# Performance work log

Measured on AMD Instinct MI355X. Metric: run time of the kernel, lower is better.

## Reference

```python
import jax, jax.numpy as jnp
import numpy as np


def setup_inputs() -> dict:
    key = jax.random.key(0)
    k1, k2 = jax.random.split(key)
    b, n, d = 8, 4096, 512
    num_codebooks, codebook_size = 1, 8192
    x = jax.random.normal(k1, (b, n, d), dtype=jnp.float32)
    embed = jax.random.normal(k2, (num_codebooks, codebook_size, d), dtype=jnp.float32)
    return {"x": x, "embed": embed}


def reference(x, embed):
    # Eval-mode forward of EuclideanCodebook (temperature 0 -> argmax of -cdist).
    # x: [b, n, d]; embed: [h, C, d] with h = num_codebooks = 1.
    b, n, d = x.shape
    h, C, _ = embed.shape
    flatten = x.reshape(h, b * n, d)                       # h * d packing (h=1)

    # dist = -cdist(flatten, embed): negative euclidean distance [h, N, C]
    x2 = jnp.sum(flatten * flatten, axis=-1, keepdims=True)   # [h, N, 1]
    e2 = jnp.sum(embed * embed, axis=-1)[:, None, :]          # [h, 1, C]
    xe = jnp.einsum('hnd,hcd->hnc', flatten, embed)           # [h, N, C]
    d2 = jnp.clip(x2 + e2 - 2.0 * xe, 0.0)
    dist = -jnp.sqrt(d2)                                      # [h, N, C]

    # gumbel_sample at temp 0 / eval -> straight argmax
    embed_ind_flat = jnp.argmax(dist, axis=-1)                # [h, N]

    # quantize = batched_embedding(embed_ind, embed): gather codes
    quantize = jnp.take_along_axis(embed, embed_ind_flat[..., None], axis=1)  # [h, N, d]

    # unpack + drop the codebook dim (needs_codebook_dim path)
    quantize = quantize.reshape(b, n, d)
    embed_ind = embed_ind_flat.reshape(b, n)
    dist = dist.reshape(h, b, n, C)  # dist keeps the codebook dim, as in source
    return quantize, embed_ind, dist
```

## Files before the change

kernel.cpp:

```cpp
#include <hip/hip_runtime.h>
#include <hip/hip_fp16.h>
#include <stdint.h>

typedef _Float16 f16x8 __attribute__((ext_vector_type(8)));
typedef _Float16 f16x4 __attribute__((ext_vector_type(4)));
typedef float    f32x4 __attribute__((ext_vector_type(4)));

static constexpr int NROWS = 32768;
static constexpr int NCODE = 8192;
static constexpr int DDIM  = 512;
static constexpr int BM = 256, BN = 256, BK = 64;
static constexpr int NBM = NROWS / BM;
static constexpr int NBN = NCODE / BN;
static constexpr int NPART = NBN * 2;

static constexpr size_t OFF_IND  = (size_t)NROWS * DDIM;
static constexpr size_t OFF_DIST = OFF_IND + NROWS;

static constexpr size_t WS_XH   = 0;
static constexpr size_t WS_XL   = WS_XH + (size_t)NROWS * DDIM * 2;
static constexpr size_t WS_EH   = WS_XL + (size_t)NROWS * DDIM * 2;
static constexpr size_t WS_EL   = WS_EH + (size_t)NCODE * DDIM * 2;
static constexpr size_t WS_X2   = WS_EL + (size_t)NCODE * DDIM * 2;
static constexpr size_t WS_E2   = WS_X2 + (size_t)NROWS * 4;
static constexpr size_t WS_PART = WS_E2 + (size_t)NCODE * 4;

__device__ inline void gload_lds16(const void* g, void* l) {
  __builtin_amdgcn_global_load_lds((const __attribute__((address_space(1))) void*)g,
                                   (__attribute__((address_space(3))) void*)l,
                                   16, 0, 0);
}

__global__ __launch_bounds__(128)
void prep_kernel(const float* __restrict__ x, const float* __restrict__ e,
                 _Float16* __restrict__ xh, _Float16* __restrict__ xl,
                 _Float16* __restrict__ eh, _Float16* __restrict__ el,
                 float* __restrict__ x2, float* __restrict__ e2)
{
  int bid = blockIdx.x;
  const float* src; _Float16 *dh, *dl; float* nrm;
  if (bid < NROWS) {
    src = x + (size_t)bid * DDIM;
    dh = xh + (size_t)bid * DDIM;  dl = xl + (size_t)bid * DDIM;
    nrm = x2 + bid;
  } else {
    int r = bid - NROWS;
    src = e + (size_t)r * DDIM;
    dh = eh + (size_t)r * DDIM;    dl = el + (size_t)r * DDIM;
    nrm = e2 + r;
  }
  int t = threadIdx.x;
  float4 v = reinterpret_cast<const float4*>(src)[t];
  double s = (double)v.x*v.x + (double)v.y*v.y + (double)v.z*v.z + (double)v.w*v.w;
  f16x4 h, l;
  h.x = (_Float16)v.x; l.x = (_Float16)(v.x - (float)h.x);
  h.y = (_Float16)v.y; l.y = (_Float16)(v.y - (float)h.y);
  h.z = (_Float16)v.z; l.z = (_Float16)(v.z - (float)h.z);
  h.w = (_Float16)v.w; l.w = (_Float16)(v.w - (float)h.w);
  reinterpret_cast<f16x4*>(dh)[t] = h;
  reinterpret_cast<f16x4*>(dl)[t] = l;
  #pragma unroll
  for (int m = 1; m < 64; m <<= 1) s += __shfl_xor(s, m);
  __shared__ double sh[2];
  if ((t & 63) == 0) sh[t >> 6] = s;
  __syncthreads();
  if (t == 0) nrm[0] = (float)(sh[0] + sh[1]);
}

#define BARx __builtin_amdgcn_s_barrier()
#define VMC(n)  asm volatile("s_waitcnt vmcnt(" #n ")" ::: "memory")

__device__ __forceinline__ void MMX(f32x4 (&ac)[2][4], const f16x8 (&af)[2][2],
                                    const f16x8 (&bf)[4][2]) {
  __builtin_amdgcn_s_setprio(1);
  #pragma unroll
  for (int m = 0; m < 2; ++m)
    #pragma unroll
    for (int n = 0; n < 4; ++n)
      #pragma unroll
      for (int ks = 0; ks < 2; ++ks)
        ac[m][n] = __builtin_amdgcn_mfma_f32_16x16x32_f16(af[m][ks], bf[n][ks], ac[m][n], 0, 0, 0);
  __builtin_amdgcn_s_setprio(0);
}

__global__ __launch_bounds__(512, 1)
void dist_gemm_kernel(const _Float16* __restrict__ xh, const _Float16* __restrict__ xl,
                      const _Float16* __restrict__ eh, const _Float16* __restrict__ el,
                      const float* __restrict__ x2, const float* __restrict__ e2,
                      float* __restrict__ dist, float2* __restrict__ part)
{
  __shared__ _Float16 L[2][2][BM * BK];

  const int tid  = threadIdx.x;
  const int wid  = tid >> 6;
  const int lane = tid & 63;
  const int qwr  = wid >> 1;
  const int qwc  = wid & 1;

  const int flat = blockIdx.x;
  const int xcd  = flat & 7;
  const int idx  = flat >> 3;
  const int bn   = xcd * 4 + (idx & 3);
  const int bm   = idx >> 2;
  const int R  = bm * BM;
  const int Cc = bn * BN;

  const int l3 = lane >> 3;
  const int l7 = lane & 7;
  const int srcslot = ((l7 ^ l3) << 4);

  auto STAGE_HALF = [&](int t, int nb, int half) {
    const int ab = half & 1;
    const int hh = half >> 1;
    const _Float16* base;
    size_t rowbase;
    if (ab == 0) { base = (t < 16) ? xh : xl;              rowbase = (size_t)R;  }
    else         { base = (t < 8 || t >= 16) ? eh : el;    rowbase = (size_t)Cc; }
    const int k0b = (t & 7) * (BK * 2);
    #pragma unroll
    for (int i = 0; i < 2; ++i) {
      const int rr = hh * 128 + wid * 16 + i * 8;
      gload_lds16((const char*)base + (rowbase + rr + l3) * (DDIM * 2) + k0b + srcslot,
                  &L[nb][ab][rr * BK]);
    }
  };

  const int l15   = lane & 15;
  const int kslot = (lane >> 4) << 4;

  auto LDA = [&](f16x8 (&af)[2][2], int b, int mq) {
    #pragma unroll
    for (int m = 0; m < 2; ++m)
      #pragma unroll
      for (int ks = 0; ks < 2; ++ks) {
        const int row = mq * 128 + qwr * 32 + m * 16 + l15;
        const int kb  = (ks * 64 + kslot) ^ ((row & 7) << 4);
        af[m][ks] = *(const f16x8*)((const char*)&L[b][0][0] + row * 128 + kb);
      }
  };
  auto LDB = [&](f16x8 (&bf)[4][2], int b, int nq) {
    #pragma unroll
    for (int n = 0; n < 4; ++n)
      #pragma unroll
      for (int ks = 0; ks < 2; ++ks) {
        const int row = nq * 128 + qwc * 64 + n * 16 + l15;
        const int kb  = (ks * 64 + kslot) ^ ((row & 7) << 4);
        bf[n][ks] = *(const f16x8*)((const char*)&L[b][1][0] + row * 128 + kb);
      }
  };

  f32x4 acc[2][2][2][4] = {};

  STAGE_HALF(0, 0, 0);
  STAGE_HALF(0, 0, 1);
  STAGE_HALF(0, 0, 2);
  STAGE_HALF(0, 0, 3);
  STAGE_HALF(1, 1, 0);
  VMC(6);
  BARx;

  for (int t = 0; t < 22; ++t) {
    const int b = t & 1;
    f16x8 af0[2][2], af1[2][2], bf0[4][2], bf1[4][2];

    LDA(af0, b, 0);  LDB(bf0, b, 0);
    STAGE_HALF(t + 1, b ^ 1, 1);
    VMC(6);  BARx;
    MMX(acc[0][0], af0, bf0);

    LDA(af1, b, 1);
    STAGE_HALF(t + 1, b ^ 1, 2);
    VMC(6);  BARx;
    MMX(acc[1][0], af1, bf0);

    LDB(bf1, b, 1);
    STAGE_HALF(t + 1, b ^ 1, 3);
    BARx;
    MMX(acc[1][1], af1, bf1);

    STAGE_HALF(t + 2, b, 0);
    VMC(6);  BARx;
    MMX(acc[0][1], af0, bf1);
  }

  {
    f16x8 af0[2][2], af1[2][2], bf0[4][2], bf1[4][2];
    LDA(af0, 0, 0);  LDB(bf0, 0, 0);
    STAGE_HALF(23, 1, 1);
    VMC(6);  BARx;
    MMX(acc[0][0], af0, bf0);
    LDA(af1, 0, 1);
    STAGE_HALF(23, 1, 2);
    VMC(6);  BARx;
    MMX(acc[1][0], af1, bf0);
    LDB(bf1, 0, 1);
    STAGE_HALF(23, 1, 3);
    BARx;
    MMX(acc[1][1], af1, bf1);
    VMC(4);  BARx;
    MMX(acc[0][1], af0, bf1);
  }
  {
    f16x8 af0[2][2], af1[2][2], bf0[4][2], bf1[4][2];
    LDA(af0, 1, 0);  LDB(bf0, 1, 0);
    VMC(2);  BARx;
    MMX(acc[0][0], af0, bf0);
    LDA(af1, 1, 1);
    VMC(0);  BARx;
    MMX(acc[1][0], af1, bf0);
    LDB(bf1, 1, 1);
    BARx;
    MMX(acc[1][1], af1, bf1);
    MMX(acc[0][1], af0, bf1);
  }

  const int q    = lane >> 4;
  const int csub = lane & 15;

  float e2v[2][4];
  #pragma unroll
  for (int nq = 0; nq < 2; ++nq)
    #pragma unroll
    for (int n = 0; n < 4; ++n)
      e2v[nq][n] = e2[Cc + nq * 128 + qwc * 64 + n * 16 + csub];

  float bestv[16], besti[16];
  int rix = 0;
  #pragma unroll
  for (int mq = 0; mq < 2; ++mq)
    #pragma unroll
    for (int m = 0; m < 2; ++m)
      #pragma unroll
      for (int j = 0; j < 4; ++j, ++rix) {
        const int row = R + mq * 128 + qwr * 32 + m * 16 + q * 4 + j;
        const float xv = x2[row];
        float* drow = dist + (size_t)row * NCODE;
        float bv = -3.0e38f, bi = 0.0f;
        #pragma unroll
        for (int nq = 0; nq < 2; ++nq)
          #pragma unroll
          for (int n = 0; n < 4; ++n) {
            const int col = Cc + nq * 128 + qwc * 64 + n * 16 + csub;
            float xe = acc[mq][nq][m][n][j];
            float d2 = fmaxf((xv + e2v[nq][n]) - 2.0f * xe, 0.0f);
            float dv = -sqrtf(d2);
            drow[col] = dv;
            if (dv > bv) { bv = dv; bi = (float)col; }
          }
        bestv[rix] = bv;
        besti[rix] = bi;
      }

  #pragma unroll
  for (int msk = 1; msk < 16; msk <<= 1) {
    #pragma unroll
    for (int r = 0; r < 16; ++r) {
      float ov = __shfl_xor(bestv[r], msk);
      float oi = __shfl_xor(besti[r], msk);
      if (ov > bestv[r] || (ov == bestv[r] && oi < besti[r])) { bestv[r] = ov; besti[r] = oi; }
    }
  }
  if (csub == 0) {
    int rr = 0;
    #pragma unroll
    for (int mq = 0; mq < 2; ++mq)
      #pragma unroll
      for (int m = 0; m < 2; ++m)
        #pragma unroll
        for (int j = 0; j < 4; ++j, ++rr) {
          const int row = R + mq * 128 + qwr * 32 + m * 16 + q * 4 + j;
          part[(size_t)row * NPART + bn * 2 + qwc] = make_float2(bestv[rr], besti[rr]);
        }
  }
}

__global__ __launch_bounds__(64)
void reduce_gather_kernel(const float2* __restrict__ part, const float* __restrict__ embed,
                          float* __restrict__ quant, float* __restrict__ ind)
{
  const int row = blockIdx.x;
  const int l = threadIdx.x;
  float2 a = part[(size_t)row * NPART + l];
  float bv = a.x, bi = a.y;
  #pragma unroll
  for (int m = 1; m < 64; m <<= 1) {
    float ov = __shfl_xor(bv, m);
    float oi = __shfl_xor(bi, m);
    if (ov > bv || (ov == bv && oi < bi)) { bv = ov; bi = oi; }
  }
  if (l == 0) ind[row] = bi;
  const int idx = (int)bi;
  const float4* src = reinterpret_cast<const float4*>(embed + (size_t)idx * DDIM);
  float4* dst = reinterpret_cast<float4*>(quant + (size_t)row * DDIM);
  dst[l]      = src[l];
  dst[l + 64] = src[l + 64];
}

extern "C" void kernel_launch(void* const* d_in, const int* in_sizes, int n_in,
                              void* d_out, int out_size, void* d_ws, size_t ws_size,
                              hipStream_t stream) {
  const float* x     = (const float*)d_in[0];
  const float* embed = (const float*)d_in[1];

  char* ws = (char*)d_ws;
  _Float16* xh = (_Float16*)(ws + WS_XH);
  _Float16* xl = (_Float16*)(ws + WS_XL);
  _Float16* eh = (_Float16*)(ws + WS_EH);
  _Float16* el = (_Float16*)(ws + WS_EL);
  float*    x2 = (float*)(ws + WS_X2);
  float*    e2 = (float*)(ws + WS_E2);
  float2*   part = (float2*)(ws + WS_PART);

  float* quant = (float*)d_out;
  float* ind   = (float*)d_out + OFF_IND;
  float* dist  = (float*)d_out + OFF_DIST;

  prep_kernel<<<dim3(NROWS + NCODE), 128, 0, stream>>>(x, embed, xh, xl, eh, el, x2, e2);
  dist_gemm_kernel<<<dim3(NBM * NBN), 512, 0, stream>>>(xh, xl, eh, el, x2, e2, dist, part);
  reduce_gather_kernel<<<dim3(NROWS), 64, 0, stream>>>(part, embed, quant, ind);
}
```

Before: 945.5 us.

## Software-pipeline LDS fragment loads across k-steps with double-buffered registers

Unrolls the main k-loop by two and keeps two register sets of A/B fragments, so the first fragments of the next k-tile are read from LDS during the last MFMA group of the current tile. Each LDS read is also issued before the MFMA that doesn't depend on it, so LDS latency overlaps with matrix math. The cost is higher VGPR pressure from the extra live fragment sets, which could reduce occupancy or cause spills.

```diff
diff --git a/kernel.cpp b/kernel.cpp
--- a/kernel.cpp
+++ b/kernel.cpp
@@ -159,59 +159,80 @@
   VMC(6);
   BARx;
 
-  for (int t = 0; t < 22; ++t) {
-    const int b = t & 1;
-    f16x8 af0[2][2], af1[2][2], bf0[4][2], bf1[4][2];
-
-    LDA(af0, b, 0);  LDB(bf0, b, 0);
-    STAGE_HALF(t + 1, b ^ 1, 1);
-    VMC(6);  BARx;
-    MMX(acc[0][0], af0, bf0);
-
-    LDA(af1, b, 1);
-    STAGE_HALF(t + 1, b ^ 1, 2);
-    VMC(6);  BARx;
-    MMX(acc[1][0], af1, bf0);
-
-    LDB(bf1, b, 1);
-    STAGE_HALF(t + 1, b ^ 1, 3);
-    BARx;
-    MMX(acc[1][1], af1, bf1);
-
-    STAGE_HALF(t + 2, b, 0);
-    VMC(6);  BARx;
-    MMX(acc[0][1], af0, bf1);
+  f16x8 afX[2][2], bfX[4][2], afY[2][2], bfY[4][2];
+  LDA(afX, 0, 0);
+  LDB(bfX, 0, 0);
+
+  for (int tt = 0; tt < 22; tt += 2) {
+    {
+      f16x8 af1[2][2], bf1[4][2];
+      STAGE_HALF(tt + 1, 1, 1);
+      VMC(6);  BARx;
+      LDA(af1, 0, 1);
+      MMX(acc[0][0], afX, bfX);
+      STAGE_HALF(tt + 1, 1, 2);
+      VMC(6);  BARx;
+      LDB(bf1, 0, 1);
+      MMX(acc[1][0], af1, bfX);
+      STAGE_HALF(tt + 1, 1, 3);
+      BARx;
+      MMX(acc[1][1], af1, bf1);
+      STAGE_HALF(tt + 2, 0, 0);
+      VMC(6);  BARx;
+      LDA(afY, 1, 0);
+      LDB(bfY, 1, 0);
+      MMX(acc[0][1], afX, bf1);
+    }
+    {
+      f16x8 af1[2][2], bf1[4][2];
+      STAGE_HALF(tt + 2, 0, 1);
+      VMC(6);  BARx;
+      LDA(af1, 1, 1);
+      MMX(acc[0][0], afY, bfY);
+      STAGE_HALF(tt + 2, 0, 2);
+      VMC(6);  BARx;
+      LDB(bf1, 1, 1);
+      MMX(acc[1][0], af1, bfY);
+      STAGE_HALF(tt + 2, 0, 3);
+      BARx;
+      MMX(acc[1][1], af1, bf1);
+      STAGE_HALF(tt + 3, 1, 0);
+      VMC(6);  BARx;
+      LDA(afX, 0, 0);
+      LDB(bfX, 0, 0);
+      MMX(acc[0][1], afY, bf1);
+    }
   }
 
   {
-    f16x8 af0[2][2], af1[2][2], bf0[4][2], bf1[4][2];
-    LDA(af0, 0, 0);  LDB(bf0, 0, 0);
+    f16x8 af1[2][2], bf1[4][2];
     STAGE_HALF(23, 1, 1);
     VMC(6);  BARx;
-    MMX(acc[0][0], af0, bf0);
     LDA(af1, 0, 1);
+    MMX(acc[0][0], afX, bfX);
     STAGE_HALF(23, 1, 2);
     VMC(6);  BARx;
-    MMX(acc[1][0], af1, bf0);
     LDB(bf1, 0, 1);
+    MMX(acc[1][0], af1, bfX);
     STAGE_HALF(23, 1, 3);
     BARx;
     MMX(acc[1][1], af1, bf1);
     VMC(4);  BARx;
-    MMX(acc[0][1], af0, bf1);
+    LDA(afY, 1, 0);
+    LDB(bfY, 1, 0);
+    MMX(acc[0][1], afX, bf1);
   }
   {
-    f16x8 af0[2][2], af1[2][2], bf0[4][2], bf1[4][2];
-    LDA(af0, 1, 0);  LDB(bf0, 1, 0);
+    f16x8 af1[2][2], bf1[4][2];
     VMC(2);  BARx;
-    MMX(acc[0][0], af0, bf0);
     LDA(af1, 1, 1);
+    MMX(acc[0][0], afY, bfY);
     VMC(0);  BARx;
-    MMX(acc[1][0], af1, bf0);
     LDB(bf1, 1, 1);
+    MMX(acc[1][0], af1, bfY);
     BARx;
     MMX(acc[1][1], af1, bf1);
-    MMX(acc[0][1], af0, bf1);
+    MMX(acc[0][1], afY, bf1);
   }
 
   const int q    = lane >> 4;
```

Result: slower. 1.891 ms (+100.0%).

## Restructure GEMM main loop to stage two halves per phase with fewer barriers

Applied to the files above, without the earlier changes.

Reschedules the double-buffered K loop of the distance GEMM. Each iteration now issues the next tile's global-to-LDS stages in two pairs, with two barrier points instead of four. All A fragments and the first B fragment are loaded in one group before the MFMAs run. The prologue and the two peeled tail iterations are folded into the loop plus a single epilogue block. The goal is less barrier and wait overhead and better grouping of LDS reads and MFMAs. The cost is a looser overlap between buffer reuse and reads, and a possible LDS write-after-read hazard on the buffer being refilled.

```diff
diff --git a/kernel.cpp b/kernel.cpp
--- a/kernel.cpp
+++ b/kernel.cpp
@@ -155,61 +155,38 @@
   STAGE_HALF(0, 0, 1);
   STAGE_HALF(0, 0, 2);
   STAGE_HALF(0, 0, 3);
-  STAGE_HALF(1, 1, 0);
-  VMC(6);
-  BARx;
-
-  for (int t = 0; t < 22; ++t) {
+
+  for (int t = 0; t < 23; ++t) {
     const int b = t & 1;
     f16x8 af0[2][2], af1[2][2], bf0[4][2], bf1[4][2];
 
-    LDA(af0, b, 0);  LDB(bf0, b, 0);
+    STAGE_HALF(t + 1, b ^ 1, 0);
     STAGE_HALF(t + 1, b ^ 1, 1);
     VMC(6);  BARx;
+    LDA(af0, b, 0);
+    LDB(bf0, b, 0);
+    LDA(af1, b, 1);
     MMX(acc[0][0], af0, bf0);
-
-    LDA(af1, b, 1);
+    MMX(acc[1][0], af1, bf0);
+
     STAGE_HALF(t + 1, b ^ 1, 2);
-    VMC(6);  BARx;
-    MMX(acc[1][0], af1, bf0);
-
+    STAGE_HALF(t + 1, b ^ 1, 3);
+    VMC(8);  BARx;
     LDB(bf1, b, 1);
-    STAGE_HALF(t + 1, b ^ 1, 3);
-    BARx;
     MMX(acc[1][1], af1, bf1);
-
-    STAGE_HALF(t + 2, b, 0);
-    VMC(6);  BARx;
     MMX(acc[0][1], af0, bf1);
   }
 
   {
     f16x8 af0[2][2], af1[2][2], bf0[4][2], bf1[4][2];
-    LDA(af0, 0, 0);  LDB(bf0, 0, 0);
-    STAGE_HALF(23, 1, 1);
-    VMC(6);  BARx;
+    VMC(2);  BARx;
+    LDA(af0, 1, 0);
+    LDB(bf0, 1, 0);
+    LDA(af1, 1, 1);
     MMX(acc[0][0], af0, bf0);
-    LDA(af1, 0, 1);
-    STAGE_HALF(23, 1, 2);
-    VMC(6);  BARx;
     MMX(acc[1][0], af1, bf0);
-    LDB(bf1, 0, 1);
-    STAGE_HALF(23, 1, 3);
-    BARx;
-    MMX(acc[1][1], af1, bf1);
-    VMC(4);  BARx;
-    MMX(acc[0][1], af0, bf1);
-  }
-  {
-    f16x8 af0[2][2], af1[2][2], bf0[4][2], bf1[4][2];
-    LDA(af0, 1, 0);  LDB(bf0, 1, 0);
-    VMC(2);  BARx;
-    MMX(acc[0][0], af0, bf0);
-    LDA(af1, 1, 1);
     VMC(0);  BARx;
-    MMX(acc[1][0], af1, bf0);
     LDB(bf1, 1, 1);
-    BARx;
     MMX(acc[1][1], af1, bf1);
     MMX(acc[0][1], af0, bf1);
   }
```

Result: no change. 956.0 us (+1.1%).
